# Performance work log

Measured on AMD Instinct MI355X. Metric: run time of the kernel, lower is better.

## Reference

```python
import jax, jax.numpy as jnp
import numpy as np

N_NODES = 500000
N_EDGES = 1000000
H = 128


def setup_inputs() -> dict:
    key = jax.random.key(0)
    ks = jax.random.split(key, 8)
    s = 1.0 / np.sqrt(H)
    return {
        "z": jax.random.normal(ks[0], (N_NODES, H), dtype=jnp.float32),
        "w1": jax.random.normal(ks[1], (H, H), dtype=jnp.float32) * s,
        "b1": jax.random.normal(ks[2], (H,), dtype=jnp.float32) * s,
        "w2": jax.random.normal(ks[3], (H, H), dtype=jnp.float32) * s,
        "b2": jax.random.normal(ks[4], (H,), dtype=jnp.float32) * s,
        "wb": jax.random.normal(ks[5], (1, H, H), dtype=jnp.float32) * s,
        "bb": jax.random.normal(ks[6], (1,), dtype=jnp.float32) * s,
        "pot_arcs": jax.random.randint(ks[7], (N_EDGES, 2), 0, N_NODES, dtype=jnp.int64),
    }


def reference(z, w1, b1, w2, b2, wb, bb, pot_arcs):
    # Gather head/dep node embeddings per candidate arc: [E, H]
    x1 = z[pot_arcs[:, 0]]
    x2 = z[pot_arcs[:, 1]]
    # Per-node linear + relu (dropout is identity in eval mode)
    h1 = jax.nn.relu(x1 @ w1.T + b1)
    h2 = jax.nn.relu(x2 @ w2.T + b2)
    # Bilinear score: h1 @ W @ h2^T per edge, out_features=1
    score = jnp.einsum("eh,hk,ek->e", h1, wb[0], h2) + bb[0]
    return score
```

## Files before the change

kernel.cpp:

```cpp
#include <hip/hip_runtime.h>
#include <hip/hip_bf16.h>

#define HDIM 128

typedef short bf16x8 __attribute__((ext_vector_type(8)));
typedef short bf16x4 __attribute__((ext_vector_type(4)));
typedef unsigned short u16x8 __attribute__((ext_vector_type(8)));
typedef float f32x4 __attribute__((ext_vector_type(4)));

__device__ __forceinline__ short f2bf(float f) {
    __hip_bfloat16 h = __float2bfloat16(f);
    union { __hip_bfloat16 h; short s; } c; c.h = h; return c.s;
}
__device__ __forceinline__ float bf2f(unsigned short h) {
    union { unsigned u; float f; } c; c.u = ((unsigned)h) << 16; return c.f;
}
__device__ __forceinline__ bf16x8 pack8(float4 a, float4 b) {
    bf16x8 r;
    r[0] = f2bf(a.x); r[1] = f2bf(a.y); r[2] = f2bf(a.z); r[3] = f2bf(a.w);
    r[4] = f2bf(b.x); r[5] = f2bf(b.y); r[6] = f2bf(b.z); r[7] = f2bf(b.w);
    return r;
}

__device__ __forceinline__ void barrier_lds() {
    asm volatile("s_waitcnt lgkmcnt(0)" ::: "memory");
    __builtin_amdgcn_s_barrier();
    __builtin_amdgcn_sched_barrier(0);
}

__global__ __launch_bounds__(512, 4)
void node_phase(const float* __restrict__ z,
                const float* __restrict__ w1, const float* __restrict__ b1,
                const float* __restrict__ w2, const float* __restrict__ b2,
                const float* __restrict__ wb,
                unsigned short* __restrict__ g1, unsigned short* __restrict__ h2o,
                int N)
{
    __shared__ short zbb[2][4096];
    __shared__ short h1x[2][4096];
    __shared__ short h2x[2][4096];
    __shared__ short g1x[2][4096];

    const int t = threadIdx.x;
    const int lane = t & 63, wid = t >> 6;
    const int l15 = lane & 15, kgrp = lane >> 4;
    const int feat = wid * 16 + l15;

    bf16x8 w1f[4], w2f[4], wbf[4];
    {
        const float* w1r = w1 + (size_t)feat * HDIM;
        const float* w2r = w2 + (size_t)feat * HDIM;
#pragma unroll
        for (int kt = 0; kt < 4; ++kt) {
            int k0 = kt * 32 + kgrp * 8;
            w1f[kt] = pack8(*(const float4*)(w1r + k0), *(const float4*)(w1r + k0 + 4));
            w2f[kt] = pack8(*(const float4*)(w2r + k0), *(const float4*)(w2r + k0 + 4));
            bf16x8 r;
#pragma unroll
            for (int i = 0; i < 8; ++i) r[i] = f2bf(wb[(size_t)(k0 + i) * HDIM + feat]);
            wbf[kt] = r;
        }
    }
    f32x4 bias1, bias2;
#pragma unroll
    for (int r = 0; r < 4; ++r) {
        bias1[r] = b1[wid * 16 + kgrp * 4 + r];
        bias2[r] = b2[wid * 16 + kgrp * 4 + r];
    }

    const int srow = t >> 4;
    const int sp   = t & 15;
    const int sg   = sp ^ (srow & 7);

    const int ntiles = (N + 31) >> 5;
    const int myTiles = (ntiles > (int)blockIdx.x)
                      ? ((ntiles - 1 - (int)blockIdx.x) / (int)gridDim.x + 1) : 0;
    const int nit = myTiles + 2;
    const int ng = wid * 2 + (kgrp >> 1);

    if (myTiles > 0) {
        int row = (int)blockIdx.x * 32 + srow;
        int rc = row < N ? row : N - 1;
        const float* src = z + (size_t)rc * HDIM + sg * 8;
        *(bf16x8*)&zbb[0][t * 8] = pack8(*(const float4*)src, *(const float4*)(src + 4));
    }
    __syncthreads();

    for (int i = 0; i < nit; ++i) {
        const int cur = i & 1, prv = cur ^ 1;
        const int tvA = (int)blockIdx.x + i * (int)gridDim.x;
        const bool vA = (i < myTiles);
        const bool vB = (i >= 1) && (i - 1 < myTiles);
        const bool vG = (i >= 2) && (i - 2 < myTiles);
        const bool vP = (i + 1 < myTiles);

        float4 zn0, zn1;
        if (vP) {
            int row = (tvA + (int)gridDim.x) * 32 + srow;
            int rc = row < N ? row : N - 1;
            const float* src = z + (size_t)rc * HDIM + sg * 8;
            zn0 = *(const float4*)src;
            zn1 = *(const float4*)(src + 4);
        }
        if (vG) {
            int row = (tvA - 2 * (int)gridDim.x) * 32 + srow;
            u16x8 vv = *(const u16x8*)&g1x[prv][srow * 128 + sp * 8];
            if (row < N) *(u16x8*)&g1[(size_t)row * HDIM + (sp ^ (srow & 7)) * 8] = vv;
        }
        if (vB) {
            int row = (tvA - (int)gridDim.x) * 32 + srow;
            u16x8 vv = *(const u16x8*)&h2x[prv][srow * 128 + sp * 8];
            if (row < N) *(u16x8*)&h2o[(size_t)row * HDIM + (sp ^ (srow & 7)) * 8] = vv;
        }
        if (vA) {
#pragma unroll
            for (int gp = 0; gp < 2; ++gp) {
                const int m = gp * 16 + l15;
                bf16x8 zf[4];
#pragma unroll
                for (int kt = 0; kt < 4; ++kt) {
                    int pos = (kt * 4 + kgrp) ^ (m & 7);
                    zf[kt] = *(const bf16x8*)&zbb[cur][m * 128 + pos * 8];
                }
                f32x4 a1 = bias1, a3 = bias2;
#pragma unroll
                for (int kt = 0; kt < 4; ++kt) {
                    a1 = __builtin_amdgcn_mfma_f32_16x16x32_bf16(w1f[kt], zf[kt], a1, 0, 0, 0);
                    a3 = __builtin_amdgcn_mfma_f32_16x16x32_bf16(w2f[kt], zf[kt], a3, 0, 0, 0);
                }
                const int sidx = m * 128 + ((ng ^ (m & 7)) << 3) + ((kgrp & 1) << 2);
                bf16x4 h1v, h2v;
#pragma unroll
                for (int r = 0; r < 4; ++r) {
                    float x1 = a1[r] > 0.f ? a1[r] : 0.f;
                    float x2 = a3[r] > 0.f ? a3[r] : 0.f;
                    h1v[r] = f2bf(x1);
                    h2v[r] = f2bf(x2);
                }
                *(bf16x4*)&h1x[cur][sidx] = h1v;
                *(bf16x4*)&h2x[cur][sidx] = h2v;
            }
        }
        if (vB) {
#pragma unroll
            for (int gp = 0; gp < 2; ++gp) {
                const int m = gp * 16 + l15;
                f32x4 ag = (f32x4){0.f, 0.f, 0.f, 0.f};
#pragma unroll
                for (int kt = 0; kt < 4; ++kt) {
                    int pos = (kt * 4 + kgrp) ^ (m & 7);
                    bf16x8 bf = *(const bf16x8*)&h1x[prv][m * 128 + pos * 8];
                    ag = __builtin_amdgcn_mfma_f32_16x16x32_bf16(wbf[kt], bf, ag, 0, 0, 0);
                }
                const int sidx = m * 128 + ((ng ^ (m & 7)) << 3) + ((kgrp & 1) << 2);
                bf16x4 gv;
#pragma unroll
                for (int r = 0; r < 4; ++r) gv[r] = f2bf(ag[r]);
                *(bf16x4*)&g1x[cur][sidx] = gv;
            }
        }
        if (vP) {
            *(bf16x8*)&zbb[prv][t * 8] = pack8(zn0, zn1);
        }
        barrier_lds();
    }
}

__global__ void detect_idx64(const int* __restrict__ arcs, int* __restrict__ flag)
{
    if (threadIdx.x == 0) {
        int is64 = 1;
        for (int j = 0; j < 64; ++j)
            if (arcs[2 * j + 1] != 0) { is64 = 0; break; }
        *flag = is64;
    }
}

__global__ __launch_bounds__(256, 8)
void edge_phase(const unsigned short* __restrict__ g1,
                const unsigned short* __restrict__ h2,
                const void* __restrict__ arcs,
                const int* __restrict__ flag,
                const float* __restrict__ bb,
                float* __restrict__ out, int E)
{
    const int t = threadIdx.x;
    const int sub = t & 15;
    const int e = blockIdx.x * 16 + (t >> 4);
    const int ec = e < E ? e : (E - 1);

    long long u, v;
    if (*flag) {
        const long long* a = (const long long*)arcs;
        u = a[2 * (size_t)ec]; v = a[2 * (size_t)ec + 1];
    } else {
        const int* a = (const int*)arcs;
        u = a[2 * (size_t)ec]; v = a[2 * (size_t)ec + 1];
    }

    u16x8 av = *(const u16x8*)(g1 + (size_t)u * HDIM + sub * 8);
    u16x8 bv = *(const u16x8*)(h2 + (size_t)v * HDIM + sub * 8);
    float s = 0.f;
#pragma unroll
    for (int i = 0; i < 8; ++i) s += bf2f(av[i]) * bf2f(bv[i]);

    s += __shfl_xor(s, 8, 16);
    s += __shfl_xor(s, 4, 16);
    s += __shfl_xor(s, 2, 16);
    s += __shfl_xor(s, 1, 16);

    if (sub == 0 && e < E) out[e] = s + bb[0];
}

extern "C" void kernel_launch(void* const* d_in, const int* in_sizes, int n_in,
                              void* d_out, int out_size, void* d_ws, size_t ws_size,
                              hipStream_t stream)
{
    const float* z  = (const float*)d_in[0];
    const float* w1 = (const float*)d_in[1];
    const float* b1 = (const float*)d_in[2];
    const float* w2 = (const float*)d_in[3];
    const float* b2 = (const float*)d_in[4];
    const float* wb = (const float*)d_in[5];
    const float* bb = (const float*)d_in[6];
    const void*  arcs = d_in[7];

    const int N = in_sizes[0] / HDIM;
    const int E = in_sizes[7] / 2;

    char* ws = (char*)d_ws;
    int* flag = (int*)ws;
    unsigned short* g1 = (unsigned short*)(ws + 256);
    unsigned short* h2 = g1 + (size_t)N * HDIM;

    detect_idx64<<<1, 64, 0, stream>>>((const int*)arcs, flag);

    node_phase<<<512, 512, 0, stream>>>(z, w1, b1, w2, b2, wb, g1, h2, N);

    int eblk = (E + 15) / 16;
    edge_phase<<<eblk, 256, 0, stream>>>(g1, h2, arcs, flag, bb, (float*)d_out, E);
}
```

Baseline: 186.9 us.

## Enlarge node tile to 64 rows and store h2/g1 directly to global

The node kernel now handles 64-row tiles instead of 32. It drops the h2x and g1x LDS staging buffers and writes the h2 and g1 MFMA outputs straight to global memory as 8-byte bf16x4 stores. This shortens the pipeline from three stages to two and removes the LDS round-trip and one stage of latency. The cost is narrower, less coalesced global stores and more registers and LDS per block. The index-width detection kernel also switches from a serial loop to a wave ballot.

```diff
diff --git a/kernel.cpp b/kernel.cpp
--- a/kernel.cpp
+++ b/kernel.cpp
@@ -36,10 +36,8 @@
                 unsigned short* __restrict__ g1, unsigned short* __restrict__ h2o,
                 int N)
 {
-    __shared__ short zbb[2][4096];
-    __shared__ short h1x[2][4096];
-    __shared__ short h2x[2][4096];
-    __shared__ short g1x[2][4096];
+    __shared__ short zbb[2][8192];
+    __shared__ short h1x[2][8192];
 
     const int t = threadIdx.x;
     const int lane = t & 63, wid = t >> 6;
@@ -68,53 +66,50 @@
         bias2[r] = b2[wid * 16 + kgrp * 4 + r];
     }
 
-    const int srow = t >> 4;
-    const int sp   = t & 15;
-    const int sg   = sp ^ (srow & 7);
-
-    const int ntiles = (N + 31) >> 5;
+    const int srow = t >> 3;
+    const int p0 = (t & 7) * 2, p1 = p0 + 1;
+    const int gA = p0 ^ (srow & 7), gB = p1 ^ (srow & 7);
+
+    const int ntiles = (N + 63) >> 6;
     const int myTiles = (ntiles > (int)blockIdx.x)
                       ? ((ntiles - 1 - (int)blockIdx.x) / (int)gridDim.x + 1) : 0;
-    const int nit = myTiles + 2;
+    const int nit = myTiles + 1;
     const int ng = wid * 2 + (kgrp >> 1);
+    const int fcol = wid * 16 + kgrp * 4;
 
     if (myTiles > 0) {
-        int row = (int)blockIdx.x * 32 + srow;
+        int row = (int)blockIdx.x * 64 + srow;
         int rc = row < N ? row : N - 1;
-        const float* src = z + (size_t)rc * HDIM + sg * 8;
-        *(bf16x8*)&zbb[0][t * 8] = pack8(*(const float4*)src, *(const float4*)(src + 4));
+        const float* src = z + (size_t)rc * HDIM;
+        *(bf16x8*)&zbb[0][srow * 128 + p0 * 8] =
+            pack8(*(const float4*)(src + gA * 8), *(const float4*)(src + gA * 8 + 4));
+        *(bf16x8*)&zbb[0][srow * 128 + p1 * 8] =
+            pack8(*(const float4*)(src + gB * 8), *(const float4*)(src + gB * 8 + 4));
     }
     __syncthreads();
 
     for (int i = 0; i < nit; ++i) {
         const int cur = i & 1, prv = cur ^ 1;
-        const int tvA = (int)blockIdx.x + i * (int)gridDim.x;
+        const int tA = (int)blockIdx.x + i * (int)gridDim.x;
         const bool vA = (i < myTiles);
-        const bool vB = (i >= 1) && (i - 1 < myTiles);
-        const bool vG = (i >= 2) && (i - 2 < myTiles);
+        const bool vB = (i >= 1);
         const bool vP = (i + 1 < myTiles);
 
-        float4 zn0, zn1;
+        float4 za0, za1, zb0, zb1;
         if (vP) {
-            int row = (tvA + (int)gridDim.x) * 32 + srow;
+            int row = (tA + (int)gridDim.x) * 64 + srow;
             int rc = row < N ? row : N - 1;
-            const float* src = z + (size_t)rc * HDIM + sg * 8;
-            zn0 = *(const float4*)src;
-            zn1 = *(const float4*)(src + 4);
-        }
-        if (vG) {
-            int row = (tvA - 2 * (int)gridDim.x) * 32 + srow;
-            u16x8 vv = *(const u16x8*)&g1x[prv][srow * 128 + sp * 8];
-            if (row < N) *(u16x8*)&g1[(size_t)row * HDIM + (sp ^ (srow & 7)) * 8] = vv;
-        }
-        if (vB) {
-            int row = (tvA - (int)gridDim.x) * 32 + srow;
-            u16x8 vv = *(const u16x8*)&h2x[prv][srow * 128 + sp * 8];
-            if (row < N) *(u16x8*)&h2o[(size_t)row * HDIM + (sp ^ (srow & 7)) * 8] = vv;
-        }
+            const float* src = z + (size_t)rc * HDIM;
+            za0 = *(const float4*)(src + gA * 8);
+            za1 = *(const float4*)(src + gA * 8 + 4);
+            zb0 = *(const float4*)(src + gB * 8);
+            zb1 = *(const float4*)(src + gB * 8 + 4);
+        }
+
         if (vA) {
-#pragma unroll
-            for (int gp = 0; gp < 2; ++gp) {
+            const int mb = tA * 64;
+#pragma unroll
+            for (int gp = 0; gp < 4; ++gp) {
                 const int m = gp * 16 + l15;
                 bf16x8 zf[4];
 #pragma unroll
@@ -128,7 +123,6 @@
                     a1 = __builtin_amdgcn_mfma_f32_16x16x32_bf16(w1f[kt], zf[kt], a1, 0, 0, 0);
                     a3 = __builtin_amdgcn_mfma_f32_16x16x32_bf16(w2f[kt], zf[kt], a3, 0, 0, 0);
                 }
-                const int sidx = m * 128 + ((ng ^ (m & 7)) << 3) + ((kgrp & 1) << 2);
                 bf16x4 h1v, h2v;
 #pragma unroll
                 for (int r = 0; r < 4; ++r) {
@@ -137,13 +131,16 @@
                     h1v[r] = f2bf(x1);
                     h2v[r] = f2bf(x2);
                 }
-                *(bf16x4*)&h1x[cur][sidx] = h1v;
-                *(bf16x4*)&h2x[cur][sidx] = h2v;
+                *(bf16x4*)&h1x[cur][m * 128 + ((ng ^ (m & 7)) << 3) + ((kgrp & 1) << 2)] = h1v;
+                int row = mb + m;
+                if (row < N) *(bf16x4*)&h2o[(size_t)row * HDIM + fcol] = h2v;
             }
         }
+
         if (vB) {
-#pragma unroll
-            for (int gp = 0; gp < 2; ++gp) {
+            const int mb = (tA - (int)gridDim.x) * 64;
+#pragma unroll
+            for (int gp = 0; gp < 4; ++gp) {
                 const int m = gp * 16 + l15;
                 f32x4 ag = (f32x4){0.f, 0.f, 0.f, 0.f};
 #pragma unroll
@@ -152,15 +149,17 @@
                     bf16x8 bf = *(const bf16x8*)&h1x[prv][m * 128 + pos * 8];
                     ag = __builtin_amdgcn_mfma_f32_16x16x32_bf16(wbf[kt], bf, ag, 0, 0, 0);
                 }
-                const int sidx = m * 128 + ((ng ^ (m & 7)) << 3) + ((kgrp & 1) << 2);
                 bf16x4 gv;
 #pragma unroll
                 for (int r = 0; r < 4; ++r) gv[r] = f2bf(ag[r]);
-                *(bf16x4*)&g1x[cur][sidx] = gv;
+                int row = mb + m;
+                if (row < N) *(bf16x4*)&g1[(size_t)row * HDIM + fcol] = gv;
             }
         }
+
         if (vP) {
-            *(bf16x8*)&zbb[prv][t * 8] = pack8(zn0, zn1);
+            *(bf16x8*)&zbb[prv][srow * 128 + p0 * 8] = pack8(za0, za1);
+            *(bf16x8*)&zbb[prv][srow * 128 + p1 * 8] = pack8(zb0, zb1);
         }
         barrier_lds();
     }
@@ -168,12 +167,9 @@
 
 __global__ void detect_idx64(const int* __restrict__ arcs, int* __restrict__ flag)
 {
-    if (threadIdx.x == 0) {
-        int is64 = 1;
-        for (int j = 0; j < 64; ++j)
-            if (arcs[2 * j + 1] != 0) { is64 = 0; break; }
-        *flag = is64;
-    }
+    int v = arcs[2 * threadIdx.x + 1];
+    unsigned long long any = __ballot(v != 0);
+    if (threadIdx.x == 0) *flag = (any == 0ull) ? 1 : 0;
 }
 
 __global__ __launch_bounds__(256, 8)
```

After: 210.1 us. +12.4%, slower.
